# Kernel tuning notes

Hardware: AMD Instinct MI355X
Metric: run time of the kernel (lower is better)

The kernel has to match this reference:

```python
import jax, jax.numpy as jnp
import numpy as np

EPS = 1e-5
ALPHA = 0.7
N_HEADS = 20
N_KV_HEADS = 5
HEAD_DIM = 128


def bitlinear(x, w):
    # absmean ternary quantization per output row: w_t = sign(w)*(|w| > alpha*absmean)
    absw = jnp.abs(w)
    absmean = jnp.mean(absw, axis=1, keepdims=True)            # [out, 1]
    tern = jnp.sign(w) * (absw > ALPHA * absmean).astype(w.dtype)
    # (X @ pos^T - X @ neg^T) * scale == (X @ tern^T) * scale
    return jnp.einsum('...i,oi->...o', x, tern) * absmean[:, 0]


def rmsnorm(x, g):
    var = jnp.mean(jnp.square(x), axis=-1, keepdims=True)
    return x * jax.lax.rsqrt(var + EPS) * g


def rotate_half(x):
    x1, x2 = jnp.split(x, 2, axis=-1)
    return jnp.concatenate([-x2, x1], axis=-1)


def setup_inputs() -> dict:
    key = jax.random.key(0)
    ks = jax.random.split(key, 12)
    h, inter = 2560, 6912
    b, s = 1, 2048
    wscale = 1.0 / np.sqrt(h)
    return {
        'x': jax.random.normal(ks[0], (b, s, h), jnp.float32),
        'cos': jax.random.uniform(ks[1], (1, 1, s, HEAD_DIM), jnp.float32),
        'sin': jax.random.uniform(ks[2], (1, 1, s, HEAD_DIM), jnp.float32),
        'q_w': jax.random.normal(ks[3], (h, h), jnp.float32) * wscale,
        'k_w': jax.random.normal(ks[4], (N_KV_HEADS * HEAD_DIM, h), jnp.float32) * wscale,
        'v_w': jax.random.normal(ks[5], (N_KV_HEADS * HEAD_DIM, h), jnp.float32) * wscale,
        'o_w': jax.random.normal(ks[6], (h, h), jnp.float32) * wscale,
        'gate_w': jax.random.normal(ks[7], (inter, h), jnp.float32) * wscale,
        'up_w': jax.random.normal(ks[8], (inter, h), jnp.float32) * wscale,
        'down_w': jax.random.normal(ks[9], (h, inter), jnp.float32) / np.sqrt(inter),
        'ln1_w': jnp.ones((h,), jnp.float32),
        'ln2_w': jnp.ones((h,), jnp.float32),
    }


def reference(x, cos, sin, q_w, k_w, v_w, o_w, gate_w, up_w, down_w, ln1_w, ln2_w):
    b, s, hdim = x.shape
    residual = x
    h = rmsnorm(x, ln1_w)

    q = bitlinear(h, q_w).reshape(b, s, N_HEADS, HEAD_DIM).transpose(0, 2, 1, 3)
    k = bitlinear(h, k_w).reshape(b, s, N_KV_HEADS, HEAD_DIM).transpose(0, 2, 1, 3)
    v = bitlinear(h, v_w).reshape(b, s, N_KV_HEADS, HEAD_DIM).transpose(0, 2, 1, 3)

    # RoPE
    q = q * cos + rotate_half(q) * sin
    k = k * cos + rotate_half(k) * sin

    # GQA: repeat_interleave kv heads
    n_rep = N_HEADS // N_KV_HEADS
    k = jnp.repeat(k, n_rep, axis=1)
    v = jnp.repeat(v, n_rep, axis=1)

    scale = 1.0 / np.sqrt(HEAD_DIM)
    attn = jnp.einsum('bhqd,bhkd->bhqk', q, k) * scale
    attn = jax.nn.softmax(attn, axis=-1)
    o = jnp.einsum('bhqk,bhkd->bhqd', attn, v)
    o = o.transpose(0, 2, 1, 3).reshape(b, s, hdim)

    x = residual + bitlinear(o, o_w)

    residual = x
    h = rmsnorm(x, ln2_w)
    gate = jnp.square(jax.nn.relu(bitlinear(h, gate_w)))  # relu^2
    x = residual + bitlinear(gate * bitlinear(h, up_w), down_w)
    return x
```

## Files before the change

kernel.cpp:

```cpp
#include <hip/hip_runtime.h>
#include <hip/hip_bf16.h>

typedef unsigned short u16;
typedef short bf16x8 __attribute__((ext_vector_type(8)));
typedef float f32x4 __attribute__((ext_vector_type(4)));
typedef float f32x16 __attribute__((ext_vector_type(16)));
typedef float f4 __attribute__((ext_vector_type(4)));
typedef unsigned short u16x4 __attribute__((ext_vector_type(4)));

__device__ __forceinline__ u16 f2b(float f) {
    union { __hip_bfloat16 h; u16 u; } cv;
    cv.h = __float2bfloat16(f);
    return cv.u;
}
__device__ __forceinline__ float b2f(u16 u) {
    union { u16 u; __hip_bfloat16 h; } cv;
    cv.u = u;
    return __bfloat162float(cv.h);
}

__device__ __forceinline__ void g2l16(const void* g, void* l) {
    __builtin_amdgcn_global_load_lds(
        (const __attribute__((address_space(1))) unsigned int*)g,
        (__attribute__((address_space(3))) unsigned int*)l, 16, 0, 0);
}

template <int NV4, int NS>
__global__ __launch_bounds__(256) void quant_kernel(const float* __restrict__ W,
                                                    u16* __restrict__ T,
                                                    float* __restrict__ scales, int K) {
    const int row = blockIdx.x, tid = threadIdx.x;
    const float* wr = W + (size_t)row * K;
    f4 v[NV4];
    float vs[NS];
    float s = 0.f;
#pragma unroll
    for (int j = 0; j < NV4; ++j) {
        v[j] = ((const f4*)wr)[tid + j * 256];
#pragma unroll
        for (int e = 0; e < 4; ++e) s += fabsf(v[j][e]);
    }
#pragma unroll
    for (int j = 0; j < NS; ++j) { vs[j] = wr[NV4 * 1024 + j * 256 + tid]; s += fabsf(vs[j]); }
#pragma unroll
    for (int d = 1; d < 64; d <<= 1) s += __shfl_xor(s, d);
    __shared__ float red[4];
    if ((tid & 63) == 0) red[tid >> 6] = s;
    __syncthreads();
    const float absmean = (red[0] + red[1] + red[2] + red[3]) / (float)K;
    const float thr = 0.7f * absmean;
    u16* tr = T + (size_t)row * K;
#pragma unroll
    for (int j = 0; j < NV4; ++j) {
        u16x4 o;
#pragma unroll
        for (int e = 0; e < 4; ++e) {
            const float w = v[j][e];
            o[e] = (fabsf(w) > thr) ? ((w > 0.f) ? (u16)0x3F80 : (u16)0xBF80) : (u16)0;
        }
        ((u16x4*)tr)[tid + j * 256] = o;
    }
#pragma unroll
    for (int j = 0; j < NS; ++j) {
        const float w = vs[j];
        tr[NV4 * 1024 + j * 256 + tid] = (fabsf(w) > thr) ? ((w > 0.f) ? (u16)0x3F80 : (u16)0xBF80) : (u16)0;
    }
    if (tid == 0) scales[row] = absmean;
}

__global__ __launch_bounds__(256) void rmsnorm_kernel(const float* __restrict__ x,
                                                      const float* __restrict__ g,
                                                      u16* __restrict__ o) {
    const int row = blockIdx.x, tid = threadIdx.x;
    const float* xr = x + (size_t)row * 2560;
    f4 v[2];
    float vs[2];
    float s = 0.f;
#pragma unroll
    for (int j = 0; j < 2; ++j) {
        v[j] = ((const f4*)xr)[tid + j * 256];
#pragma unroll
        for (int e = 0; e < 4; ++e) s += v[j][e] * v[j][e];
    }
#pragma unroll
    for (int j = 0; j < 2; ++j) { vs[j] = xr[2048 + j * 256 + tid]; s += vs[j] * vs[j]; }
#pragma unroll
    for (int d = 1; d < 64; d <<= 1) s += __shfl_xor(s, d);
    __shared__ float red[4];
    if ((tid & 63) == 0) red[tid >> 6] = s;
    __syncthreads();
    const float total = red[0] + red[1] + red[2] + red[3];
    const float rs = rsqrtf(total * (1.f / 2560.f) + 1e-5f);
    u16* orow = o + (size_t)row * 2560;
#pragma unroll
    for (int j = 0; j < 2; ++j) {
        const f4 gv = ((const f4*)g)[tid + j * 256];
        u16x4 ov;
#pragma unroll
        for (int e = 0; e < 4; ++e) ov[e] = f2b(v[j][e] * rs * gv[e]);
        ((u16x4*)orow)[tid + j * 256] = ov;
    }
#pragma unroll
    for (int j = 0; j < 2; ++j)
        orow[2048 + j * 256 + tid] = f2b(vs[j] * rs * g[2048 + j * 256 + tid]);
}

template <int MODE>
__global__ __launch_bounds__(512, 4) void gemm_bt(const u16* __restrict__ A,
                                                  const u16* __restrict__ B,
                                                  const float* __restrict__ scale,
                                                  const float* res,
                                                  void* __restrict__ outp,
                                                  int M, int N, int K) {
    __shared__ __align__(16) u16 sA[2][128 * 64];
    __shared__ __align__(16) u16 sB[2][128 * 64];
    const int tid = threadIdx.x;
    const int wave = tid >> 6, lane = tid & 63;
    const int l31 = lane & 31, half = lane >> 5;

    const int nwg = gridDim.x * gridDim.y;
    int lin = blockIdx.y * gridDim.x + blockIdx.x;
    lin = (lin & 7) * (nwg >> 3) + (lin >> 3);
    const int m0 = (lin % gridDim.x) * 128, n0 = (lin / gridDim.x) * 128;
    const int wm = wave >> 2, wn = wave & 3;

    f32x16 acc[2] = {};

    const int r0 = wave * 8 + (lane >> 3);
    const int gcc = (lane & 7) ^ (lane >> 3);
    const size_t aoff = (size_t)(m0 + r0) * K + gcc * 8;
    const size_t boff = (size_t)(n0 + r0) * K + gcc * 8;
    const int swz = l31 & 7;
    const int arow0 = (wm * 64 + l31) * 64;
    const int arow1 = (wm * 64 + 32 + l31) * 64;
    const int brow = (wn * 32 + l31) * 64;

    auto stage = [&](int kt, int b) {
        char* ldsA = (char*)(&sA[b][0]) + wave * 1024;
        char* ldsB = (char*)(&sB[b][0]) + wave * 1024;
        g2l16(A + aoff + kt, ldsA);
        g2l16(A + aoff + (size_t)64 * K + kt, ldsA + 8192);
        g2l16(B + boff + kt, ldsB);
        g2l16(B + boff + (size_t)64 * K + kt, ldsB + 8192);
    };

    stage(0, 0);
    __syncthreads();
    const int nk = K >> 6;
    for (int t = 0; t < nk; ++t) {
        const int buf = t & 1;
        if (t + 1 < nk) stage((t + 1) * 64, buf ^ 1);
        const u16* pA = &sA[buf][0];
        const u16* pB = &sB[buf][0];
#pragma unroll
        for (int ks = 0; ks < 4; ++ks) {
            const int pc = ((ks * 2 + half) ^ swz) * 8;
            const bf16x8 bfr = *(const bf16x8*)&pB[brow + pc];
            const bf16x8 a0 = *(const bf16x8*)&pA[arow0 + pc];
            const bf16x8 a1 = *(const bf16x8*)&pA[arow1 + pc];
            acc[0] = __builtin_amdgcn_mfma_f32_32x32x16_bf16(a0, bfr, acc[0], 0, 0, 0);
            acc[1] = __builtin_amdgcn_mfma_f32_32x32x16_bf16(a1, bfr, acc[1], 0, 0, 0);
        }
        __syncthreads();
    }

    const int c = n0 + wn * 32 + l31;
    const float sc = scale[c];
#pragma unroll
    for (int mt = 0; mt < 2; ++mt) {
        const int rb = m0 + wm * 64 + mt * 32 + 4 * half;
#pragma unroll
        for (int r = 0; r < 16; ++r) {
            const int row = rb + (r & 3) + 8 * (r >> 2);
            const float vv = acc[mt][r] * sc;
            const size_t idx = (size_t)row * N + c;
            if (MODE == 0)      ((u16*)outp)[idx] = f2b(vv);
            else if (MODE == 1) ((float*)outp)[idx] = res[idx] + vv;
            else {
                const float gg = fmaxf(b2f(((const u16*)res)[idx]), 0.f);
                ((u16*)outp)[idx] = f2b(gg * gg * vv);
            }
        }
    }
}

__global__ __launch_bounds__(256) void rope_kernel(u16* __restrict__ buf, int stride,
                                                   const float* __restrict__ cs,
                                                   const float* __restrict__ sn, int nh) {
    const int idx = blockIdx.x * 256 + threadIdx.x;
    const int d = idx & 63;
    const int h = (idx >> 6) % nh;
    const int s = idx / (64 * nh);
    const size_t base = (size_t)s * stride + h * 128;
    const float a = b2f(buf[base + d]), b = b2f(buf[base + d + 64]);
    const float c1 = cs[s * 128 + d], s1 = sn[s * 128 + d];
    const float c2 = cs[s * 128 + d + 64], s2 = sn[s * 128 + d + 64];
    buf[base + d] = f2b(a * c1 - b * s1);
    buf[base + d + 64] = f2b(b * c2 + a * s2);
}

__global__ __launch_bounds__(256) void transpose_v_kernel(const u16* __restrict__ V, int stride,
                                                          u16* __restrict__ VT) {
    __shared__ u16 t[128 * 66];
    const int tid = threadIdx.x;
    const int h = blockIdx.y, s0 = blockIdx.x * 64;
#pragma unroll
    for (int i = 0; i < 32; ++i) {
        const int idx = tid + i * 256;
        const int r = idx >> 7, c = idx & 127;
        t[c * 66 + r] = V[(size_t)(s0 + r) * stride + h * 128 + c];
    }
    __syncthreads();
#pragma unroll
    for (int i = 0; i < 32; ++i) {
        const int idx = tid + i * 256;
        const int d = idx >> 6, s = idx & 63;
        VT[((size_t)h * 128 + d) * 2048 + s0 + s] = t[d * 66 + s];
    }
}

__global__ __launch_bounds__(256, 3) void flash_kernel(const u16* __restrict__ Q, int qs,
                                                       const u16* __restrict__ Kb,
                                                       const u16* __restrict__ VT,
                                                       u16* __restrict__ O) {
    __shared__ __align__(16) u16 sQ[64 * 128];
    __shared__ __align__(16) u16 sK[2][32 * 128];
    __shared__ __align__(16) u16 sV[2][128 * 32];
    const int tid = threadIdx.x, wave = tid >> 6, lane = tid & 63;
    const int lane15 = lane & 15, quad = lane >> 4;
    int lin = blockIdx.y * 32 + blockIdx.x;
    lin = (lin & 7) * 80 + (lin >> 3);
    const int head = lin >> 5, q0 = (lin & 31) * 64, kvh = head >> 2;
    const int sw = lane15 & 7;

    const int rk = wave * 4 + (lane >> 4);
    const int gk = (lane & 15) ^ (rk & 7);
    const u16* kbase = Kb + (size_t)rk * qs + kvh * 128 + gk * 8;
    const int rv = wave * 16 + (lane >> 2);
    const int gv = (lane & 3) ^ ((lane >> 3) & 3);
    const u16* vbase = VT + ((size_t)kvh * 128 + rv) * 2048 + gv * 8;

    auto stage = [&](int k0, int b) {
        char* dK = (char*)(&sK[b][0]) + wave * 1024;
        char* dV = (char*)(&sV[b][0]) + wave * 1024;
#pragma unroll
        for (int s = 0; s < 2; ++s) {
            g2l16(kbase + ((size_t)k0 + s * 16) * qs, dK + s * 4096);
            g2l16(vbase + (size_t)s * 64 * 2048 + k0, dV + s * 4096);
        }
    };

    {
        const int rq = wave * 4 + (lane >> 4);
        const int gq = (lane & 15) ^ (rq & 7);
        const u16* src = Q + (size_t)(q0 + rq) * qs + head * 128 + gq * 8;
        char* dst = (char*)sQ + wave * 1024;
#pragma unroll
        for (int s = 0; s < 4; ++s)
            g2l16(src + (size_t)s * 16 * qs, dst + s * 4096);
        stage(0, 0);
    }
    __syncthreads();
    bf16x8 qf[4];
#pragma unroll
    for (int kc = 0; kc < 4; ++kc)
        qf[kc] = *(const bf16x8*)&sQ[(wave * 16 + lane15) * 128 + ((kc * 4 + quad) ^ sw) * 8];

    float m_i[4], lp[4];
    f32x4 o_acc[8] = {};
#pragma unroll
    for (int r = 0; r < 4; ++r) { m_i[r] = -1e30f; lp[r] = 0.f; }

    const float sl2e = 0.088388347648318447f * 1.4426950408889634f;
    const float THR = 8.0f;
    u16* sP = sQ;

    for (int t = 0; t < 64; ++t) {
        const int buf = t & 1;
        if (t < 63) stage((t + 1) * 32, buf ^ 1);
        const u16* sKb = &sK[buf][0];
        const u16* sVb = &sV[buf][0];

        f32x4 sacc[2] = {};
        __builtin_amdgcn_s_setprio(1);
#pragma unroll
        for (int nf = 0; nf < 2; ++nf)
#pragma unroll
            for (int kc = 0; kc < 4; ++kc) {
                const bf16x8 kf = *(const bf16x8*)&sKb[(nf * 16 + lane15) * 128 + ((kc * 4 + quad) ^ sw) * 8];
                sacc[nf] = __builtin_amdgcn_mfma_f32_16x16x32_bf16(qf[kc], kf, sacc[nf], 0, 0, 0);
            }
        __builtin_amdgcn_s_setprio(0);

        float mx[4];
#pragma unroll
        for (int r = 0; r < 4; ++r) {
            float v0 = sacc[0][r] * sl2e, v1 = sacc[1][r] * sl2e;
            sacc[0][r] = v0; sacc[1][r] = v1;
            float m0 = fmaxf(v0, v1);
#pragma unroll
            for (int d = 1; d < 16; d <<= 1) m0 = fmaxf(m0, __shfl_xor(m0, d));
            mx[r] = m0;
        }
        const int upd = (mx[0] > m_i[0] + THR) | (mx[1] > m_i[1] + THR) |
                        (mx[2] > m_i[2] + THR) | (mx[3] > m_i[3] + THR);
        if (__any(upd)) {
#pragma unroll
            for (int r = 0; r < 4; ++r) {
                const float mnew = fmaxf(m_i[r], mx[r]);
                const float alpha = exp2f(m_i[r] - mnew);
                m_i[r] = mnew;
                lp[r] *= alpha;
#pragma unroll
                for (int nf = 0; nf < 8; ++nf) o_acc[nf][r] *= alpha;
            }
        }
#pragma unroll
        for (int r = 0; r < 4; ++r) {
            const float m = m_i[r];
            const float p0 = exp2f(sacc[0][r] - m), p1 = exp2f(sacc[1][r] - m);
            sacc[0][r] = p0; sacc[1][r] = p1;
            lp[r] += p0 + p1;
        }

#pragma unroll
        for (int nf = 0; nf < 2; ++nf) {
            const int pcol = nf * 16 + lane15;
#pragma unroll
            for (int r = 0; r < 4; ++r)
                sP[(wave * 16 + quad * 4 + r) * 40 + pcol] = f2b(sacc[nf][r]);
        }

        const bf16x8 pf = *(const bf16x8*)&sP[(wave * 16 + lane15) * 40 + quad * 8];
        __builtin_amdgcn_s_setprio(1);
#pragma unroll
        for (int nf = 0; nf < 8; ++nf) {
            const bf16x8 vf = *(const bf16x8*)&sVb[(nf * 16 + lane15) * 32 +
                                                   ((quad ^ ((lane15 >> 1) & 3))) * 8];
            o_acc[nf] = __builtin_amdgcn_mfma_f32_16x16x32_bf16(pf, vf, o_acc[nf], 0, 0, 0);
        }
        __builtin_amdgcn_s_setprio(0);
        __syncthreads();
    }

#pragma unroll
    for (int r = 0; r < 4; ++r) {
        float lt = lp[r];
#pragma unroll
        for (int d = 1; d < 16; d <<= 1) lt += __shfl_xor(lt, d);
        const float inv = 1.f / lt;
        const int row = q0 + wave * 16 + quad * 4 + r;
        u16* orow = O + (size_t)row * 2560 + head * 128;
#pragma unroll
        for (int nf = 0; nf < 8; ++nf)
            orow[nf * 16 + lane15] = f2b(o_acc[nf][r] * inv);
    }
}

extern "C" void kernel_launch(void* const* d_in, const int* in_sizes, int n_in,
                              void* d_out, int out_size, void* d_ws, size_t ws_size,
                              hipStream_t stream) {
    (void)in_sizes; (void)n_in; (void)out_size; (void)ws_size;
    const float* x      = (const float*)d_in[0];
    const float* cosb   = (const float*)d_in[1];
    const float* sinb   = (const float*)d_in[2];
    const float* q_w    = (const float*)d_in[3];
    const float* k_w    = (const float*)d_in[4];
    const float* v_w    = (const float*)d_in[5];
    const float* o_w    = (const float*)d_in[6];
    const float* gate_w = (const float*)d_in[7];
    const float* up_w   = (const float*)d_in[8];
    const float* down_w = (const float*)d_in[9];
    const float* ln1    = (const float*)d_in[10];
    const float* ln2    = (const float*)d_in[11];

    char* w = (char*)d_ws;
    size_t off = 0;
    auto nxt = [&](size_t sz) { char* p = w + off; off += sz; return p; };
    u16*   TQ = (u16*)nxt(13107200);
    u16*   TK = (u16*)nxt(3276800);
    u16*   TV = (u16*)nxt(3276800);
    u16*   TO = (u16*)nxt(13107200);
    u16*   TB = (u16*)nxt(35389440);
    float* SC = (float*)nxt(91136);
    u16*   H  = (u16*)nxt(10485760);
    u16*   QKV = (u16*)nxt(15728640);
    u16*   VT = (u16*)nxt(2621440);
    float* XM = (float*)nxt(20971520);
    u16*   G  = (u16*)nxt(28311552);

    quant_kernel<2, 2><<<2560, 256, 0, stream>>>(q_w, TQ, SC + 0, 2560);
    quant_kernel<2, 2><<<640, 256, 0, stream>>>(k_w, TK, SC + 2560, 2560);
    quant_kernel<2, 2><<<640, 256, 0, stream>>>(v_w, TV, SC + 3200, 2560);
    quant_kernel<2, 2><<<2560, 256, 0, stream>>>(o_w, TO, SC + 3840, 2560);
    rmsnorm_kernel<<<2048, 256, 0, stream>>>(x, ln1, H);
    gemm_bt<0><<<dim3(16, 30), 512, 0, stream>>>(H, TQ, SC + 0, nullptr, QKV, 2048, 3840, 2560);
    rope_kernel<<<10240, 256, 0, stream>>>(QKV, 3840, cosb, sinb, 20);
    rope_kernel<<<2560, 256, 0, stream>>>(QKV + 2560, 3840, cosb, sinb, 5);
    transpose_v_kernel<<<dim3(32, 5), 256, 0, stream>>>(QKV + 3200, 3840, VT);
    flash_kernel<<<dim3(32, 20), 256, 0, stream>>>(QKV, 3840, QKV + 2560, VT, H);
    gemm_bt<1><<<dim3(16, 20), 512, 0, stream>>>(H, TO, SC + 3840, x, XM, 2048, 2560, 2560);

    rmsnorm_kernel<<<2048, 256, 0, stream>>>(XM, ln2, H);
    quant_kernel<2, 2><<<6912, 256, 0, stream>>>(gate_w, TB, SC + 6400, 2560);
    gemm_bt<0><<<dim3(16, 54), 512, 0, stream>>>(H, TB, SC + 6400, nullptr, G, 2048, 6912, 2560);
    quant_kernel<2, 2><<<6912, 256, 0, stream>>>(up_w, TB, SC + 13312, 2560);
    gemm_bt<2><<<dim3(16, 54), 512, 0, stream>>>(H, TB, SC + 13312, (const float*)G, G, 2048, 6912, 2560);
    quant_kernel<6, 3><<<2560, 256, 0, stream>>>(down_w, TB, SC + 20224, 6912);
    gemm_bt<1><<<dim3(16, 20), 512, 0, stream>>>(G, TB, SC + 20224, XM, (float*)d_out, 2048, 2560, 6912);
}
```

Before: 863.4 us.

## Deepen GEMM prefetch pipeline, use wave-per-row quantization, drop flash block swizzle

The GEMM main loop now keeps two K-tiles in flight, using explicit vmcnt waits and raw s_barrier calls in place of a single-stage prefetch with __syncthreads. The goal is to overlap global-to-LDS loads with MFMA compute. The quantization kernel now handles one row per wave with a shuffle-only reduction and re-reads the weights instead of holding them in registers, which removes the LDS reduction and block sync. The flash kernel drops its XCD-aware block remapping in favor of direct blockIdx indexing, which may reduce L2 locality for K/V.

```diff
diff --git a/kernel.cpp b/kernel.cpp
--- a/kernel.cpp
+++ b/kernel.cpp
@@ -25,47 +25,34 @@
         (__attribute__((address_space(3))) unsigned int*)l, 16, 0, 0);
 }
 
-template <int NV4, int NS>
+template <int NF4>
 __global__ __launch_bounds__(256) void quant_kernel(const float* __restrict__ W,
                                                     u16* __restrict__ T,
                                                     float* __restrict__ scales, int K) {
-    const int row = blockIdx.x, tid = threadIdx.x;
+    const int wid = threadIdx.x >> 6, lane = threadIdx.x & 63;
+    const int row = blockIdx.x * 4 + wid;
     const float* wr = W + (size_t)row * K;
-    f4 v[NV4];
-    float vs[NS];
     float s = 0.f;
 #pragma unroll
-    for (int j = 0; j < NV4; ++j) {
-        v[j] = ((const f4*)wr)[tid + j * 256];
-#pragma unroll
-        for (int e = 0; e < 4; ++e) s += fabsf(v[j][e]);
-    }
-#pragma unroll
-    for (int j = 0; j < NS; ++j) { vs[j] = wr[NV4 * 1024 + j * 256 + tid]; s += fabsf(vs[j]); }
+    for (int j = 0; j < NF4; ++j) {
+        const f4 v = ((const f4*)wr)[lane + j * 64];
+        s += fabsf(v[0]) + fabsf(v[1]) + fabsf(v[2]) + fabsf(v[3]);
+    }
 #pragma unroll
     for (int d = 1; d < 64; d <<= 1) s += __shfl_xor(s, d);
-    __shared__ float red[4];
-    if ((tid & 63) == 0) red[tid >> 6] = s;
-    __syncthreads();
-    const float absmean = (red[0] + red[1] + red[2] + red[3]) / (float)K;
+    const float absmean = s / (float)K;
     const float thr = 0.7f * absmean;
     u16* tr = T + (size_t)row * K;
 #pragma unroll
-    for (int j = 0; j < NV4; ++j) {
+    for (int j = 0; j < NF4; ++j) {
+        const f4 v = ((const f4*)wr)[lane + j * 64];
         u16x4 o;
 #pragma unroll
-        for (int e = 0; e < 4; ++e) {
-            const float w = v[j][e];
-            o[e] = (fabsf(w) > thr) ? ((w > 0.f) ? (u16)0x3F80 : (u16)0xBF80) : (u16)0;
-        }
-        ((u16x4*)tr)[tid + j * 256] = o;
-    }
-#pragma unroll
-    for (int j = 0; j < NS; ++j) {
-        const float w = vs[j];
-        tr[NV4 * 1024 + j * 256 + tid] = (fabsf(w) > thr) ? ((w > 0.f) ? (u16)0x3F80 : (u16)0xBF80) : (u16)0;
-    }
-    if (tid == 0) scales[row] = absmean;
+        for (int e = 0; e < 4; ++e)
+            o[e] = (fabsf(v[e]) > thr) ? ((v[e] > 0.f) ? (u16)0x3F80 : (u16)0xBF80) : (u16)0;
+        ((u16x4*)tr)[lane + j * 64] = o;
+    }
+    if (lane == 0) scales[row] = absmean;
 }
 
 __global__ __launch_bounds__(256) void rmsnorm_kernel(const float* __restrict__ x,
@@ -136,22 +123,16 @@
     const int brow = (wn * 32 + l31) * 64;
 
     auto stage = [&](int kt, int b) {
-        char* ldsA = (char*)(&sA[b][0]) + wave * 1024;
-        char* ldsB = (char*)(&sB[b][0]) + wave * 1024;
-        g2l16(A + aoff + kt, ldsA);
-        g2l16(A + aoff + (size_t)64 * K + kt, ldsA + 8192);
-        g2l16(B + boff + kt, ldsB);
-        g2l16(B + boff + (size_t)64 * K + kt, ldsB + 8192);
+        char* la = (char*)(&sA[b][0]) + wave * 1024;
+        char* lb = (char*)(&sB[b][0]) + wave * 1024;
+        g2l16(A + aoff + kt, la);
+        g2l16(A + aoff + (size_t)64 * K + kt, la + 8192);
+        g2l16(B + boff + kt, lb);
+        g2l16(B + boff + (size_t)64 * K + kt, lb + 8192);
     };
-
-    stage(0, 0);
-    __syncthreads();
-    const int nk = K >> 6;
-    for (int t = 0; t < nk; ++t) {
-        const int buf = t & 1;
-        if (t + 1 < nk) stage((t + 1) * 64, buf ^ 1);
-        const u16* pA = &sA[buf][0];
-        const u16* pB = &sB[buf][0];
+    auto compute = [&](int b) {
+        const u16* pA = &sA[b][0];
+        const u16* pB = &sB[b][0];
 #pragma unroll
         for (int ks = 0; ks < 4; ++ks) {
             const int pc = ((ks * 2 + half) ^ swz) * 8;
@@ -161,8 +142,25 @@
             acc[0] = __builtin_amdgcn_mfma_f32_32x32x16_bf16(a0, bfr, acc[0], 0, 0, 0);
             acc[1] = __builtin_amdgcn_mfma_f32_32x32x16_bf16(a1, bfr, acc[1], 0, 0, 0);
         }
-        __syncthreads();
-    }
+    };
+
+    const int nk = K >> 6;
+    stage(0, 0);
+    stage(64, 1);
+    for (int t = 0; t < nk - 1; ++t) {
+        asm volatile("s_waitcnt vmcnt(4)" ::: "memory");
+        __builtin_amdgcn_sched_barrier(0);
+        __builtin_amdgcn_s_barrier();
+        compute(t & 1);
+        asm volatile("s_waitcnt lgkmcnt(0)" ::: "memory");
+        __builtin_amdgcn_sched_barrier(0);
+        __builtin_amdgcn_s_barrier();
+        if (t + 2 < nk) stage((t + 2) * 64, t & 1);
+    }
+    asm volatile("s_waitcnt vmcnt(0)" ::: "memory");
+    __builtin_amdgcn_sched_barrier(0);
+    __builtin_amdgcn_s_barrier();
+    compute((nk - 1) & 1);
 
     const int c = n0 + wn * 32 + l31;
     const float sc = scale[c];
@@ -228,9 +226,7 @@
     __shared__ __align__(16) u16 sV[2][128 * 32];
     const int tid = threadIdx.x, wave = tid >> 6, lane = tid & 63;
     const int lane15 = lane & 15, quad = lane >> 4;
-    int lin = blockIdx.y * 32 + blockIdx.x;
-    lin = (lin & 7) * 80 + (lin >> 3);
-    const int head = lin >> 5, q0 = (lin & 31) * 64, kvh = head >> 2;
+    const int head = blockIdx.y, q0 = blockIdx.x * 64, kvh = head >> 2;
     const int sw = lane15 & 7;
 
     const int rk = wave * 4 + (lane >> 4);
@@ -389,10 +385,10 @@
     float* XM = (float*)nxt(20971520);
     u16*   G  = (u16*)nxt(28311552);
 
-    quant_kernel<2, 2><<<2560, 256, 0, stream>>>(q_w, TQ, SC + 0, 2560);
-    quant_kernel<2, 2><<<640, 256, 0, stream>>>(k_w, TK, SC + 2560, 2560);
-    quant_kernel<2, 2><<<640, 256, 0, stream>>>(v_w, TV, SC + 3200, 2560);
-    quant_kernel<2, 2><<<2560, 256, 0, stream>>>(o_w, TO, SC + 3840, 2560);
+    quant_kernel<10><<<640, 256, 0, stream>>>(q_w, TQ, SC + 0, 2560);
+    quant_kernel<10><<<160, 256, 0, stream>>>(k_w, TK, SC + 2560, 2560);
+    quant_kernel<10><<<160, 256, 0, stream>>>(v_w, TV, SC + 3200, 2560);
+    quant_kernel<10><<<640, 256, 0, stream>>>(o_w, TO, SC + 3840, 2560);
     rmsnorm_kernel<<<2048, 256, 0, stream>>>(x, ln1, H);
     gemm_bt<0><<<dim3(16, 30), 512, 0, stream>>>(H, TQ, SC + 0, nullptr, QKV, 2048, 3840, 2560);
     rope_kernel<<<10240, 256, 0, stream>>>(QKV, 3840, cosb, sinb, 20);
@@ -402,10 +398,10 @@
     gemm_bt<1><<<dim3(16, 20), 512, 0, stream>>>(H, TO, SC + 3840, x, XM, 2048, 2560, 2560);
 
     rmsnorm_kernel<<<2048, 256, 0, stream>>>(XM, ln2, H);
-    quant_kernel<2, 2><<<6912, 256, 0, stream>>>(gate_w, TB, SC + 6400, 2560);
+    quant_kernel<10><<<1728, 256, 0, stream>>>(gate_w, TB, SC + 6400, 2560);
     gemm_bt<0><<<dim3(16, 54), 512, 0, stream>>>(H, TB, SC + 6400, nullptr, G, 2048, 6912, 2560);
-    quant_kernel<2, 2><<<6912, 256, 0, stream>>>(up_w, TB, SC + 13312, 2560);
+    quant_kernel<10><<<1728, 256, 0, stream>>>(up_w, TB, SC + 13312, 2560);
     gemm_bt<2><<<dim3(16, 54), 512, 0, stream>>>(H, TB, SC + 13312, (const float*)G, G, 2048, 6912, 2560);
-    quant_kernel<6, 3><<<2560, 256, 0, stream>>>(down_w, TB, SC + 20224, 6912);
+    quant_kernel<27><<<640, 256, 0, stream>>>(down_w, TB, SC + 20224, 6912);
     gemm_bt<1><<<dim3(16, 20), 512, 0, stream>>>(G, TB, SC + 20224, XM, (float*)d_out, 2048, 2560, 6912);
 }
```

Measured after the change: 857.8 us. About the same (-0.6%).
